# Optimization experiments

Hardware: AMD Instinct MI355X
Metric: run time of the kernel (lower is better)

The kernel has to match this reference:

```python
import jax, jax.numpy as jnp
import numpy as np


def setup_inputs() -> dict:
    key = jax.random.key(0)
    k1, k2, k3, k4, k5 = jax.random.split(key, 5)
    N, T, D, H = 64, 512, 512, 512
    std = 1.0 / np.sqrt(H)
    return {
        "x": jax.random.normal(k1, (N, T, D), dtype=jnp.float32),
        "weight_xh": jax.random.uniform(k2, (D, 4 * H), jnp.float32, -std, std),
        "weight_hh": jax.random.uniform(k3, (H, 4 * H), jnp.float32, -std, std),
        "bias_xh": jax.random.uniform(k4, (4 * H,), jnp.float32, -std, std),
        "bias_hh": jax.random.uniform(k5, (4 * H,), jnp.float32, -std, std),
    }


def reference(x, weight_xh, weight_hh, bias_xh, bias_hh):
    # x: (N, T, D) -> (T, N, D)
    x = jnp.transpose(x, (1, 0, 2))
    T, N, _ = x.shape
    H = weight_hh.shape[0]
    # Input projection for all timesteps at once: (T, N, 4H)
    xh = jnp.einsum("tnd,dk->tnk", x, weight_xh) + bias_xh

    def step(carry, xh_t):
        h_prev, c_prev = carry
        gates = xh_t + h_prev @ weight_hh + bias_hh  # (N, 4H)
        i = jax.nn.sigmoid(gates[:, 0:H])
        f = jax.nn.sigmoid(gates[:, H:2 * H])
        g = jnp.tanh(gates[:, 2 * H:3 * H])
        o = jax.nn.sigmoid(gates[:, 3 * H:4 * H])
        c = f * c_prev + i * g
        h = o * jnp.tanh(c)
        return (h, c), h

    h0 = jnp.zeros((N, H), dtype=x.dtype)
    c0 = jnp.zeros((N, H), dtype=x.dtype)
    _, y = jax.lax.scan(step, (h0, c0), xh)  # y: (T, N, H)
    return jnp.transpose(y, (1, 0, 2))  # (N, T, H)
```

## Files before the change

kernel.cpp:

```cpp
#include <hip/hip_runtime.h>

typedef unsigned short u16;
typedef unsigned int   u32;
typedef unsigned long long u64;
typedef __attribute__((ext_vector_type(8))) short short8;
typedef __attribute__((ext_vector_type(4))) float f32x4;

#define NB   64
#define TS   512
#define HD   512
#define RG   4
#define CG   16
#define NBLK (RG*CG)
#define HROW 256
#define SLOT (NB*HROW)

__device__ __forceinline__ u16 f2bf(float x) {
    union { float f; u32 i; } v; v.f = x;
    u32 r = (v.i + 0x7fffu + ((v.i >> 16) & 1u)) >> 16;
    return (u16)r;
}
__device__ __forceinline__ u32 pack2bf(float a, float b) {
    return (u32)f2bf(a) | ((u32)f2bf(b) << 16);
}
__device__ __forceinline__ float sigmf(float x) { return 1.0f / (1.0f + __expf(-x)); }
__device__ __forceinline__ float tanhf_fast(float x) { return 1.0f - 2.0f / (__expf(2.0f * x) + 1.0f); }

__global__ void cvt_x_k(const float* __restrict__ in, u16* __restrict__ out, int n) {
    int i = (blockIdx.x * blockDim.x + threadIdx.x) * 8;
    const int stride = gridDim.x * blockDim.x * 8;
    for (; i < n; i += stride) {
        const f32x4 a = *(const f32x4*)(in + i);
        const f32x4 b = *(const f32x4*)(in + i + 4);
        u32 q[4];
        q[0] = pack2bf(a[0], a[1]);
        q[1] = pack2bf(a[2], a[3]);
        q[2] = pack2bf(b[0], b[1]);
        q[3] = pack2bf(b[2], b[3]);
        *(f32x4*)(out + i) = *(f32x4*)q;
    }
}

__global__ void transpose_cvt_k(const float* __restrict__ in, u16* __restrict__ out,
                                int R, int C) {
    __shared__ float tile[32][33];
    const int c0 = blockIdx.x * 32;
    const int r0 = blockIdx.y * 32;
    const int tx = threadIdx.x & 31;
    const int ty = threadIdx.x >> 5;
#pragma unroll
    for (int i = 0; i < 32; i += 8)
        tile[ty + i][tx] = in[(size_t)(r0 + ty + i) * C + c0 + tx];
    __syncthreads();
#pragma unroll
    for (int i = 0; i < 32; i += 8)
        out[(size_t)(c0 + ty + i) * R + r0 + tx] = f2bf(tile[tx][ty + i]);
}

__global__ __launch_bounds__(512, 2) void lstm_fused(
    const u16*   __restrict__ xbg,
    const u16*   __restrict__ WtX,
    const u16*   __restrict__ WtH,
    const float* __restrict__ bxh,
    const float* __restrict__ bhh,
    u64*   __restrict__ hbuf,
    float* __restrict__ y)
{
    const int bid  = blockIdx.x;
    const int r    = bid & 3;
    const int cg   = bid >> 2;
    const int tid  = threadIdx.x;
    const int lane = tid & 63;
    const int wv   = tid >> 6;
    const int g    = wv & 3;
    const int kh   = wv >> 2;
    const int m15  = lane & 15;
    const int kq   = lane >> 4;
    const int n0   = r * 16;
    const int gcol0 = g * 512 + cg * 32;
    const int kbase = kh * 256;

    __shared__ __align__(16) u32 ldsH[16 * 256];
    __shared__ float gbuf2[2][4][16][34];

    short8 wx[2][8], wh[2][8];
#pragma unroll
    for (int c = 0; c < 2; ++c) {
        const u16* px = WtX + (size_t)(gcol0 + c * 16 + m15) * 512 + kbase + kq * 8;
        const u16* ph = WtH + (size_t)(gcol0 + c * 16 + m15) * 512 + kbase + kq * 8;
#pragma unroll
        for (int kc = 0; kc < 8; ++kc) {
            wx[c][kc] = *(const short8*)(px + kc * 32);
            wh[c][kc] = *(const short8*)(ph + kc * 32);
        }
    }

    const int erow = tid >> 5;
    const int ecol = tid & 31;
    const int hcol = cg * 32 + ecol;
    const float bI = bxh[hcol]        + bhh[hcol];
    const float bF = bxh[512  + hcol] + bhh[512  + hcol];
    const float bG = bxh[1024 + hcol] + bhh[1024 + hcol];
    const float bO = bxh[1536 + hcol] + bhh[1536 + hcol];
    float cst = 0.0f;

    const int lrow = 2 * wv + (lane >> 5);
    const int lq   = lane & 31;
    const int swzw = (lrow & 7) << 2;

    short8 xb[8];
    {
        const u16* xg = xbg + (size_t)(n0 + m15) * TS * HD + kbase + kq * 8;
#pragma unroll
        for (int kc = 0; kc < 8; ++kc) xb[kc] = *(const short8*)(xg + kc * 32);
    }

    for (int t = 0; t < TS; ++t) {
        u64 hq[8];
        const u64* gsrc = hbuf + (size_t)((t - 1) & 3) * SLOT
                        + (size_t)(n0 + lrow) * HROW + lq;
        if (t > 0) {
#pragma unroll
            for (int i = 0; i < 8; ++i)
                hq[i] = __hip_atomic_load(gsrc + i * 32, __ATOMIC_RELAXED,
                                          __HIP_MEMORY_SCOPE_AGENT);
        }

        f32x4 a00 = {0.f,0.f,0.f,0.f}, a01 = {0.f,0.f,0.f,0.f};
        f32x4 a10 = {0.f,0.f,0.f,0.f}, a11 = {0.f,0.f,0.f,0.f};
#pragma unroll
        for (int kc = 0; kc < 8; kc += 2) {
            a00 = __builtin_amdgcn_mfma_f32_16x16x32_bf16(xb[kc],   wx[0][kc],   a00, 0, 0, 0);
            a10 = __builtin_amdgcn_mfma_f32_16x16x32_bf16(xb[kc],   wx[1][kc],   a10, 0, 0, 0);
            a01 = __builtin_amdgcn_mfma_f32_16x16x32_bf16(xb[kc+1], wx[0][kc+1], a01, 0, 0, 0);
            a11 = __builtin_amdgcn_mfma_f32_16x16x32_bf16(xb[kc+1], wx[1][kc+1], a11, 0, 0, 0);
        }

        if (t > 0) {
            const u32 tagv = (u32)t;
            for (;;) {
                u32 stale = 0;
#pragma unroll
                for (int i = 0; i < 8; ++i) stale |= ((u32)hq[i]) ^ tagv;
                if (__all(stale == 0)) break;
                __builtin_amdgcn_s_sleep(1);
#pragma unroll
                for (int i = 0; i < 8; ++i)
                    hq[i] = __hip_atomic_load(gsrc + i * 32, __ATOMIC_RELAXED,
                                              __HIP_MEMORY_SCOPE_AGENT);
            }
#pragma unroll
            for (int i = 0; i < 8; ++i)
                ldsH[lrow * 256 + ((i * 32 + lq) ^ swzw)] = (u32)(hq[i] >> 32);
            __syncthreads();

            const u32* lbase = ldsH + m15 * 256;
            const int swzr = (m15 & 7) << 2;
#pragma unroll
            for (int kc = 0; kc < 8; kc += 2) {
                short8 h0 = *(const short8*)(lbase + (((kbase >> 1) + kc * 16 + kq * 4) ^ swzr));
                short8 h1 = *(const short8*)(lbase + (((kbase >> 1) + (kc + 1) * 16 + kq * 4) ^ swzr));
                a00 = __builtin_amdgcn_mfma_f32_16x16x32_bf16(h0, wh[0][kc],   a00, 0, 0, 0);
                a10 = __builtin_amdgcn_mfma_f32_16x16x32_bf16(h0, wh[1][kc],   a10, 0, 0, 0);
                a01 = __builtin_amdgcn_mfma_f32_16x16x32_bf16(h1, wh[0][kc+1], a01, 0, 0, 0);
                a11 = __builtin_amdgcn_mfma_f32_16x16x32_bf16(h1, wh[1][kc+1], a11, 0, 0, 0);
            }
        }

        {
            const f32x4 s0 = a00 + a01;
            const f32x4 s1 = a10 + a11;
#pragma unroll
            for (int j = 0; j < 4; ++j) {
                gbuf2[kh][g][kq * 4 + j][m15]      = s0[j];
                gbuf2[kh][g][kq * 4 + j][16 + m15] = s1[j];
            }
        }
        __syncthreads();

        {
            const float gi = gbuf2[0][0][erow][ecol] + gbuf2[1][0][erow][ecol] + bI;
            const float gf = gbuf2[0][1][erow][ecol] + gbuf2[1][1][erow][ecol] + bF;
            const float gg = gbuf2[0][2][erow][ecol] + gbuf2[1][2][erow][ecol] + bG;
            const float go = gbuf2[0][3][erow][ecol] + gbuf2[1][3][erow][ecol] + bO;
            const float iv = sigmf(gi);
            const float fv = sigmf(gf);
            const float gv = tanhf_fast(gg);
            const float ov = sigmf(go);
            cst = fv * cst + iv * gv;
            const float hv = ov * tanhf_fast(cst);
            y[((size_t)(n0 + erow) * TS + t) * HD + hcol] = hv;

            const u32 me = (u32)f2bf(hv);
            const u32 nb = (u32)__shfl_xor((int)me, 1);
            if ((ecol & 1) == 0) {
                const u64 v = ((u64)(me | (nb << 16)) << 32) | (u64)(u32)(t + 1);
                __hip_atomic_store(hbuf + (size_t)(t & 3) * SLOT
                                   + (size_t)(n0 + erow) * HROW + cg * 16 + (ecol >> 1),
                                   v, __ATOMIC_RELAXED, __HIP_MEMORY_SCOPE_AGENT);
            }
        }

        if (t + 1 < TS) {
            const u16* xg = xbg + ((size_t)(n0 + m15) * TS + (t + 1)) * HD + kbase + kq * 8;
#pragma unroll
            for (int kc = 0; kc < 8; ++kc) xb[kc] = *(const short8*)(xg + kc * 32);
        }
    }
}

extern "C" void kernel_launch(void* const* d_in, const int* in_sizes, int n_in,
                              void* d_out, int out_size, void* d_ws, size_t ws_size,
                              hipStream_t stream) {
    const float* x   = (const float*)d_in[0];
    const float* wxh = (const float*)d_in[1];
    const float* whh = (const float*)d_in[2];
    const float* bxh = (const float*)d_in[3];
    const float* bhh = (const float*)d_in[4];
    float* y = (float*)d_out;

    char* ws = (char*)d_ws;
    u64* hbuf = (u64*)ws;
    u16* WtX  = (u16*)(ws + (size_t)(1 << 19));
    u16* WtH  = (u16*)(ws + (size_t)(1 << 19) + (size_t)2048 * 512 * 2);
    u16* xbg  = (u16*)(ws + (size_t)(1 << 19) + (size_t)2 * 2048 * 512 * 2);

    (void)hipMemsetAsync(hbuf, 0, (size_t)4 * SLOT * sizeof(u64), stream);

    cvt_x_k<<<2048, 256, 0, stream>>>(x, xbg, NB * TS * HD);

    dim3 tgrid(2048 / 32, 512 / 32);
    transpose_cvt_k<<<tgrid, 256, 0, stream>>>(wxh, WtX, 512, 2048);
    transpose_cvt_k<<<tgrid, 256, 0, stream>>>(whh, WtH, 512, 2048);

    lstm_fused<<<dim3(NBLK), dim3(512), 0, stream>>>(xbg, WtX, WtH, bxh, bhh,
                                                     hbuf, y);
}
```

Measured before the change: 1.957 ms.

## Co-locate each batch-row chain on one XCC and poll hidden state through local cache

Launches an oversized grid of 1024 blocks. Each block reads its XCC id and claims a slot, so that each group of 16 column blocks sharing a batch-row chain sits on the same XCC; surplus blocks exit early. Producers also store h with sc0, and consumers poll with sc0 loads (a fast mode probed at t=1, with a periodic agent-scope fallback) to cut cross-die coherence latency on the per-step exchange. An epoch counter folded into the tags keeps stale buffers from earlier launches from matching. In exchange it adds block-claim overhead, extra stores and memsets, and relies on the XCC placement of co-resident blocks.

```diff
diff --git a/kernel.cpp b/kernel.cpp
--- a/kernel.cpp
+++ b/kernel.cpp
@@ -11,9 +11,10 @@
 #define HD   512
 #define RG   4
 #define CG   16
-#define NBLK (RG*CG)
+#define NGRID 1024
 #define HROW 256
 #define SLOT (NB*HROW)
+#define XCC_SIMM (20 | (3 << 11))
 
 __device__ __forceinline__ u16 f2bf(float x) {
     union { float f; u32 i; } v; v.f = x;
@@ -57,6 +58,39 @@
         out[(size_t)(c0 + ty + i) * R + r0 + tx] = f2bf(tile[tx][ty + i]);
 }
 
+__global__ void epoch_k(u32* e) {
+    __hip_atomic_fetch_add(e, 1u, __ATOMIC_RELAXED, __HIP_MEMORY_SCOPE_AGENT);
+}
+
+#define LOAD8_SC0(hq, p)                                                      \
+    asm volatile(                                                             \
+        "global_load_dwordx2 %0, %8, off sc0\n\t"                             \
+        "global_load_dwordx2 %1, %8, off offset:256 sc0\n\t"                  \
+        "global_load_dwordx2 %2, %8, off offset:512 sc0\n\t"                  \
+        "global_load_dwordx2 %3, %8, off offset:768 sc0\n\t"                  \
+        "global_load_dwordx2 %4, %8, off offset:1024 sc0\n\t"                 \
+        "global_load_dwordx2 %5, %8, off offset:1280 sc0\n\t"                 \
+        "global_load_dwordx2 %6, %8, off offset:1536 sc0\n\t"                 \
+        "global_load_dwordx2 %7, %8, off offset:1792 sc0\n\t"                 \
+        "s_waitcnt vmcnt(0)"                                                  \
+        : "=&v"(hq[0]), "=&v"(hq[1]), "=&v"(hq[2]), "=&v"(hq[3]),             \
+          "=&v"(hq[4]), "=&v"(hq[5]), "=&v"(hq[6]), "=&v"(hq[7])              \
+        : "v"(p) : "memory")
+
+__device__ __forceinline__ void load8_agent(u64* hq, const u64* p) {
+#pragma unroll
+    for (int i = 0; i < 8; ++i)
+        hq[i] = __hip_atomic_load(p + i * 32, __ATOMIC_RELAXED,
+                                  __HIP_MEMORY_SCOPE_AGENT);
+}
+
+__device__ __forceinline__ u32 tagmiss(const u64* hq, u32 tagv) {
+    u32 stale = 0;
+#pragma unroll
+    for (int i = 0; i < 8; ++i) stale |= ((u32)hq[i]) ^ tagv;
+    return stale;
+}
+
 __global__ __launch_bounds__(512, 2) void lstm_fused(
     const u16*   __restrict__ xbg,
     const u16*   __restrict__ WtX,
@@ -64,12 +98,47 @@
     const float* __restrict__ bxh,
     const float* __restrict__ bhh,
     u64*   __restrict__ hbuf,
-    float* __restrict__ y)
+    float* __restrict__ y,
+    u32*   __restrict__ epoch,
+    u32*   __restrict__ ctrl)
 {
-    const int bid  = blockIdx.x;
-    const int r    = bid & 3;
-    const int cg   = bid >> 2;
     const int tid  = threadIdx.x;
+    __shared__ u32 sClaim[3];
+    __shared__ __align__(16) u32 ldsH[16 * 256];
+    __shared__ float gbuf2[2][4][16][34];
+
+    if (tid == 0) {
+        const u32 key = __builtin_amdgcn_s_getreg(XCC_SIMM) & 7u;
+        u32* keySlot  = ctrl;
+        u32* chainCnt = ctrl + 8;
+        u32* chainTbl = ctrl + 16;
+        const u32 slot = __hip_atomic_fetch_add(keySlot + key, 1u,
+                                                __ATOMIC_RELAXED, __HIP_MEMORY_SCOPE_AGENT);
+        const u32 grp  = slot >> 4;
+        u32* entry = chainTbl + key * 64 + grp;
+        u32 ch;
+        if ((slot & 15u) == 0u) {
+            const u32 c = __hip_atomic_fetch_add(chainCnt, 1u,
+                                                 __ATOMIC_RELAXED, __HIP_MEMORY_SCOPE_AGENT);
+            ch = (c < RG) ? (c + 1u) : 0xFFFFFFFFu;
+            __hip_atomic_store(entry, ch, __ATOMIC_RELAXED, __HIP_MEMORY_SCOPE_AGENT);
+        } else {
+            do {
+                ch = __hip_atomic_load(entry, __ATOMIC_RELAXED, __HIP_MEMORY_SCOPE_AGENT);
+            } while (ch == 0u);
+        }
+        sClaim[0] = ch;
+        sClaim[1] = slot & 15u;
+        sClaim[2] = __hip_atomic_load(epoch, __ATOMIC_RELAXED, __HIP_MEMORY_SCOPE_AGENT);
+    }
+    __syncthreads();
+    const u32 chv = sClaim[0];
+    if (chv == 0xFFFFFFFFu) return;
+
+    const int r    = (int)chv - 1;
+    const int cg   = (int)sClaim[1];
+    const u32 tagbase = sClaim[2] << 10;
+
     const int lane = tid & 63;
     const int wv   = tid >> 6;
     const int g    = wv & 3;
@@ -80,9 +149,6 @@
     const int gcol0 = g * 512 + cg * 32;
     const int kbase = kh * 256;
 
-    __shared__ __align__(16) u32 ldsH[16 * 256];
-    __shared__ float gbuf2[2][4][16][34];
-
     short8 wx[2][8], wh[2][8];
 #pragma unroll
     for (int c = 0; c < 2; ++c) {
@@ -115,16 +181,13 @@
         for (int kc = 0; kc < 8; ++kc) xb[kc] = *(const short8*)(xg + kc * 32);
     }
 
+    int fastm = 0;
+
     for (int t = 0; t < TS; ++t) {
         u64 hq[8];
         const u64* gsrc = hbuf + (size_t)((t - 1) & 3) * SLOT
                         + (size_t)(n0 + lrow) * HROW + lq;
-        if (t > 0) {
-#pragma unroll
-            for (int i = 0; i < 8; ++i)
-                hq[i] = __hip_atomic_load(gsrc + i * 32, __ATOMIC_RELAXED,
-                                          __HIP_MEMORY_SCOPE_AGENT);
-        }
+        if (t > 0 && !fastm) load8_agent(hq, gsrc);
 
         f32x4 a00 = {0.f,0.f,0.f,0.f}, a01 = {0.f,0.f,0.f,0.f};
         f32x4 a10 = {0.f,0.f,0.f,0.f}, a11 = {0.f,0.f,0.f,0.f};
@@ -137,17 +200,34 @@
         }
 
         if (t > 0) {
-            const u32 tagv = (u32)t;
-            for (;;) {
-                u32 stale = 0;
-#pragma unroll
-                for (int i = 0; i < 8; ++i) stale |= ((u32)hq[i]) ^ tagv;
-                if (__all(stale == 0)) break;
-                __builtin_amdgcn_s_sleep(1);
-#pragma unroll
-                for (int i = 0; i < 8; ++i)
-                    hq[i] = __hip_atomic_load(gsrc + i * 32, __ATOMIC_RELAXED,
-                                              __HIP_MEMORY_SCOPE_AGENT);
+            const u32 tagv = tagbase | (u32)t;
+            if (fastm) {
+                int spins = 0;
+                for (;;) {
+                    LOAD8_SC0(hq, gsrc);
+                    if (__all(tagmiss(hq, tagv) == 0u)) break;
+                    ++spins;
+                    if ((spins & 255) == 0) {
+                        load8_agent(hq, gsrc);
+                        if (__all(tagmiss(hq, tagv) == 0u)) { fastm = 0; break; }
+                    }
+                    if (spins > 8) __builtin_amdgcn_s_sleep(1);
+                }
+            } else {
+                int spins = 0;
+                while (!__all(tagmiss(hq, tagv) == 0u)) {
+                    if (++spins > 4) __builtin_amdgcn_s_sleep(1);
+                    load8_agent(hq, gsrc);
+                }
+                if (t == 1) {
+                    u64 hp[8];
+                    int ok = 0;
+                    for (int pr = 0; pr < 8 && !ok; ++pr) {
+                        LOAD8_SC0(hp, gsrc);
+                        ok = __all(tagmiss(hp, tagv) == 0u);
+                    }
+                    fastm = ok;
+                }
             }
 #pragma unroll
             for (int i = 0; i < 8; ++i)
@@ -192,12 +272,15 @@
             y[((size_t)(n0 + erow) * TS + t) * HD + hcol] = hv;
 
             const u32 me = (u32)f2bf(hv);
-            const u32 nb = (u32)__shfl_xor((int)me, 1);
+            const u32 nb2 = (u32)__shfl_xor((int)me, 1);
             if ((ecol & 1) == 0) {
-                const u64 v = ((u64)(me | (nb << 16)) << 32) | (u64)(u32)(t + 1);
-                __hip_atomic_store(hbuf + (size_t)(t & 3) * SLOT
-                                   + (size_t)(n0 + erow) * HROW + cg * 16 + (ecol >> 1),
-                                   v, __ATOMIC_RELAXED, __HIP_MEMORY_SCOPE_AGENT);
+                const u64 v = ((u64)(me | (nb2 << 16)) << 32)
+                            | (u64)(tagbase | (u32)(t + 1));
+                u64* dst = hbuf + (size_t)(t & 3) * SLOT
+                         + (size_t)(n0 + erow) * HROW + cg * 16 + (ecol >> 1);
+                __hip_atomic_store(dst, v, __ATOMIC_RELAXED, __HIP_MEMORY_SCOPE_AGENT);
+                asm volatile("global_store_dwordx2 %0, %1, off sc0"
+                             :: "v"(dst), "v"(v) : "memory");
             }
         }
 
@@ -220,12 +303,16 @@
     float* y = (float*)d_out;
 
     char* ws = (char*)d_ws;
-    u64* hbuf = (u64*)ws;
-    u16* WtX  = (u16*)(ws + (size_t)(1 << 19));
-    u16* WtH  = (u16*)(ws + (size_t)(1 << 19) + (size_t)2048 * 512 * 2);
-    u16* xbg  = (u16*)(ws + (size_t)(1 << 19) + (size_t)2 * 2048 * 512 * 2);
-
-    (void)hipMemsetAsync(hbuf, 0, (size_t)4 * SLOT * sizeof(u64), stream);
+    u32* epoch = (u32*)ws;
+    u32* ctrl  = (u32*)(ws + 256);
+    u64* hbuf  = (u64*)(ws + 8192);
+    u16* WtX   = (u16*)(ws + 8192 + (size_t)4 * SLOT * 8);
+    u16* WtH   = (u16*)((char*)WtX + (size_t)2048 * 512 * 2);
+    u16* xbg   = (u16*)((char*)WtH + (size_t)2048 * 512 * 2);
+
+    epoch_k<<<1, 1, 0, stream>>>(epoch);
+    (void)hipMemsetAsync(ctrl, 0, 4096, stream);
+    (void)hipMemsetAsync(hbuf, 0, (size_t)4 * SLOT * 8, stream);
 
     cvt_x_k<<<2048, 256, 0, stream>>>(x, xbg, NB * TS * HD);
 
@@ -233,6 +320,6 @@
     transpose_cvt_k<<<tgrid, 256, 0, stream>>>(wxh, WtX, 512, 2048);
     transpose_cvt_k<<<tgrid, 256, 0, stream>>>(whh, WtH, 512, 2048);
 
-    lstm_fused<<<dim3(NBLK), dim3(512), 0, stream>>>(xbg, WtX, WtH, bxh, bhh,
-                                                     hbuf, y);
-}
+    lstm_fused<<<dim3(NGRID), dim3(512), 0, stream>>>(xbg, WtX, WtH, bxh, bhh,
+                                                      hbuf, y, epoch, ctrl);
+}
```

Result: slower. 2.267 ms (+15.8%).

## Restructure LSTM step so gates stay in registers and hbuf poll is prefetched

Applied to the files above, without the earlier changes.

Reorders the weight rows so each lane's MFMA output holds the i/f/g/o gates of the same hidden unit. This lets the elementwise LSTM update run directly on accumulators instead of going through an LDS gate buffer and an extra block barrier. Half the waves now issue the next step's hbuf poll loads early and pass partial sums through LDS behind a per-wave flag. The hidden-state LDS buffer is double-buffered so each step needs one barrier. An epoch counter is added to the tags so stale hbuf entries from earlier launches cannot match, at the cost of extra spin-wait logic and an added kernel launch.

```diff
diff --git a/kernel.cpp b/kernel.cpp
--- a/kernel.cpp
+++ b/kernel.cpp
@@ -57,6 +57,23 @@
         out[(size_t)(c0 + ty + i) * R + r0 + tx] = f2bf(tile[tx][ty + i]);
 }
 
+__global__ void epoch_k(u32* e) {
+    __hip_atomic_fetch_add(e, 1u, __ATOMIC_RELAXED, __HIP_MEMORY_SCOPE_AGENT);
+}
+
+__device__ __forceinline__ void load16_agent(u64* hq, const u64* p) {
+#pragma unroll
+    for (int i = 0; i < 16; ++i)
+        hq[i] = __hip_atomic_load(p + i * 16, __ATOMIC_RELAXED,
+                                  __HIP_MEMORY_SCOPE_AGENT);
+}
+__device__ __forceinline__ u32 tagmiss16(const u64* hq, u32 tagv) {
+    u32 stale = 0;
+#pragma unroll
+    for (int i = 0; i < 16; ++i) stale |= ((u32)hq[i]) ^ tagv;
+    return stale;
+}
+
 __global__ __launch_bounds__(512, 2) void lstm_fused(
     const u16*   __restrict__ xbg,
     const u16*   __restrict__ WtX,
@@ -64,7 +81,8 @@
     const float* __restrict__ bxh,
     const float* __restrict__ bhh,
     u64*   __restrict__ hbuf,
-    float* __restrict__ y)
+    float* __restrict__ y,
+    u32*   __restrict__ epoch)
 {
     const int bid  = blockIdx.x;
     const int r    = bid & 3;
@@ -72,41 +90,52 @@
     const int tid  = threadIdx.x;
     const int lane = tid & 63;
     const int wv   = tid >> 6;
-    const int g    = wv & 3;
+    const int p    = wv & 3;
     const int kh   = wv >> 2;
     const int m15  = lane & 15;
     const int kq   = lane >> 4;
     const int n0   = r * 16;
-    const int gcol0 = g * 512 + cg * 32;
     const int kbase = kh * 256;
 
-    __shared__ __align__(16) u32 ldsH[16 * 256];
-    __shared__ float gbuf2[2][4][16][34];
+    __shared__ __align__(16) u32 ldsH[2][16 * 256];
+    __shared__ f32x4 pbufA[4][64];
+    __shared__ f32x4 pbufB[4][64];
+    __shared__ u32 pflag[4];
+    __shared__ u32 sEpoch;
+
+    if (tid == 0)
+        sEpoch = __hip_atomic_load(epoch, __ATOMIC_RELAXED, __HIP_MEMORY_SCOPE_AGENT);
+    if (tid < 4) pflag[tid] = 0;
+    __syncthreads();
+    const u32 tagbase = sEpoch << 10;
 
     short8 wx[2][8], wh[2][8];
 #pragma unroll
-    for (int c = 0; c < 2; ++c) {
-        const u16* px = WtX + (size_t)(gcol0 + c * 16 + m15) * 512 + kbase + kq * 8;
-        const u16* ph = WtH + (size_t)(gcol0 + c * 16 + m15) * 512 + kbase + kq * 8;
+    for (int tt = 0; tt < 2; ++tt) {
+        const int gcolA = (m15 & 3) * 512 + cg * 32 + 8 * p + 4 * tt + (m15 >> 2);
+        const u16* px = WtX + (size_t)gcolA * 512 + kbase + kq * 8;
+        const u16* ph = WtH + (size_t)gcolA * 512 + kbase + kq * 8;
 #pragma unroll
         for (int kc = 0; kc < 8; ++kc) {
-            wx[c][kc] = *(const short8*)(px + kc * 32);
-            wh[c][kc] = *(const short8*)(ph + kc * 32);
-        }
-    }
-
-    const int erow = tid >> 5;
-    const int ecol = tid & 31;
-    const int hcol = cg * 32 + ecol;
-    const float bI = bxh[hcol]        + bhh[hcol];
-    const float bF = bxh[512  + hcol] + bhh[512  + hcol];
-    const float bG = bxh[1024 + hcol] + bhh[1024 + hcol];
-    const float bO = bxh[1536 + hcol] + bhh[1536 + hcol];
-    float cst = 0.0f;
-
-    const int lrow = 2 * wv + (lane >> 5);
-    const int lq   = lane & 31;
-    const int swzw = (lrow & 7) << 2;
+            wx[tt][kc] = *(const short8*)(px + kc * 32);
+            wh[tt][kc] = *(const short8*)(ph + kc * 32);
+        }
+    }
+
+    const int hc0 = cg * 32 + 8 * p + kq;
+    const float bI0 = bxh[hc0]        + bhh[hc0];
+    const float bF0 = bxh[512 + hc0]  + bhh[512 + hc0];
+    const float bG0 = bxh[1024 + hc0] + bhh[1024 + hc0];
+    const float bO0 = bxh[1536 + hc0] + bhh[1536 + hc0];
+    const float bI1 = bxh[hc0 + 4]        + bhh[hc0 + 4];
+    const float bF1 = bxh[512 + hc0 + 4]  + bhh[512 + hc0 + 4];
+    const float bG1 = bxh[1024 + hc0 + 4] + bhh[1024 + hc0 + 4];
+    const float bO1 = bxh[1536 + hc0 + 4] + bhh[1536 + hc0 + 4];
+    float c0st = 0.0f, c1st = 0.0f;
+
+    const int lrow4 = 4 * p + (lane >> 4);
+    const int lq    = lane & 15;
+    const int swzP  = (lrow4 & 7) << 2;
 
     short8 xb[8];
     {
@@ -115,96 +144,106 @@
         for (int kc = 0; kc < 8; ++kc) xb[kc] = *(const short8*)(xg + kc * 32);
     }
 
+    u64 hq[16];
+
     for (int t = 0; t < TS; ++t) {
-        u64 hq[8];
-        const u64* gsrc = hbuf + (size_t)((t - 1) & 3) * SLOT
-                        + (size_t)(n0 + lrow) * HROW + lq;
-        if (t > 0) {
-#pragma unroll
-            for (int i = 0; i < 8; ++i)
-                hq[i] = __hip_atomic_load(gsrc + i * 32, __ATOMIC_RELAXED,
-                                          __HIP_MEMORY_SCOPE_AGENT);
-        }
-
-        f32x4 a00 = {0.f,0.f,0.f,0.f}, a01 = {0.f,0.f,0.f,0.f};
-        f32x4 a10 = {0.f,0.f,0.f,0.f}, a11 = {0.f,0.f,0.f,0.f};
+        f32x4 A00 = {0.f,0.f,0.f,0.f}, A01 = {0.f,0.f,0.f,0.f};
+        f32x4 A10 = {0.f,0.f,0.f,0.f}, A11 = {0.f,0.f,0.f,0.f};
 #pragma unroll
         for (int kc = 0; kc < 8; kc += 2) {
-            a00 = __builtin_amdgcn_mfma_f32_16x16x32_bf16(xb[kc],   wx[0][kc],   a00, 0, 0, 0);
-            a10 = __builtin_amdgcn_mfma_f32_16x16x32_bf16(xb[kc],   wx[1][kc],   a10, 0, 0, 0);
-            a01 = __builtin_amdgcn_mfma_f32_16x16x32_bf16(xb[kc+1], wx[0][kc+1], a01, 0, 0, 0);
-            a11 = __builtin_amdgcn_mfma_f32_16x16x32_bf16(xb[kc+1], wx[1][kc+1], a11, 0, 0, 0);
-        }
-
-        if (t > 0) {
-            const u32 tagv = (u32)t;
-            for (;;) {
-                u32 stale = 0;
-#pragma unroll
-                for (int i = 0; i < 8; ++i) stale |= ((u32)hq[i]) ^ tagv;
-                if (__all(stale == 0)) break;
-                __builtin_amdgcn_s_sleep(1);
-#pragma unroll
-                for (int i = 0; i < 8; ++i)
-                    hq[i] = __hip_atomic_load(gsrc + i * 32, __ATOMIC_RELAXED,
-                                              __HIP_MEMORY_SCOPE_AGENT);
-            }
-#pragma unroll
-            for (int i = 0; i < 8; ++i)
-                ldsH[lrow * 256 + ((i * 32 + lq) ^ swzw)] = (u32)(hq[i] >> 32);
-            __syncthreads();
-
-            const u32* lbase = ldsH + m15 * 256;
-            const int swzr = (m15 & 7) << 2;
-#pragma unroll
-            for (int kc = 0; kc < 8; kc += 2) {
-                short8 h0 = *(const short8*)(lbase + (((kbase >> 1) + kc * 16 + kq * 4) ^ swzr));
-                short8 h1 = *(const short8*)(lbase + (((kbase >> 1) + (kc + 1) * 16 + kq * 4) ^ swzr));
-                a00 = __builtin_amdgcn_mfma_f32_16x16x32_bf16(h0, wh[0][kc],   a00, 0, 0, 0);
-                a10 = __builtin_amdgcn_mfma_f32_16x16x32_bf16(h0, wh[1][kc],   a10, 0, 0, 0);
-                a01 = __builtin_amdgcn_mfma_f32_16x16x32_bf16(h1, wh[0][kc+1], a01, 0, 0, 0);
-                a11 = __builtin_amdgcn_mfma_f32_16x16x32_bf16(h1, wh[1][kc+1], a11, 0, 0, 0);
-            }
-        }
-
-        {
-            const f32x4 s0 = a00 + a01;
-            const f32x4 s1 = a10 + a11;
-#pragma unroll
-            for (int j = 0; j < 4; ++j) {
-                gbuf2[kh][g][kq * 4 + j][m15]      = s0[j];
-                gbuf2[kh][g][kq * 4 + j][16 + m15] = s1[j];
-            }
-        }
-        __syncthreads();
-
-        {
-            const float gi = gbuf2[0][0][erow][ecol] + gbuf2[1][0][erow][ecol] + bI;
-            const float gf = gbuf2[0][1][erow][ecol] + gbuf2[1][1][erow][ecol] + bF;
-            const float gg = gbuf2[0][2][erow][ecol] + gbuf2[1][2][erow][ecol] + bG;
-            const float go = gbuf2[0][3][erow][ecol] + gbuf2[1][3][erow][ecol] + bO;
-            const float iv = sigmf(gi);
-            const float fv = sigmf(gf);
-            const float gv = tanhf_fast(gg);
-            const float ov = sigmf(go);
-            cst = fv * cst + iv * gv;
-            const float hv = ov * tanhf_fast(cst);
-            y[((size_t)(n0 + erow) * TS + t) * HD + hcol] = hv;
-
-            const u32 me = (u32)f2bf(hv);
-            const u32 nb = (u32)__shfl_xor((int)me, 1);
-            if ((ecol & 1) == 0) {
-                const u64 v = ((u64)(me | (nb << 16)) << 32) | (u64)(u32)(t + 1);
-                __hip_atomic_store(hbuf + (size_t)(t & 3) * SLOT
-                                   + (size_t)(n0 + erow) * HROW + cg * 16 + (ecol >> 1),
-                                   v, __ATOMIC_RELAXED, __HIP_MEMORY_SCOPE_AGENT);
-            }
+            A00 = __builtin_amdgcn_mfma_f32_16x16x32_bf16(wx[0][kc],   xb[kc],   A00, 0, 0, 0);
+            A10 = __builtin_amdgcn_mfma_f32_16x16x32_bf16(wx[1][kc],   xb[kc],   A10, 0, 0, 0);
+            A01 = __builtin_amdgcn_mfma_f32_16x16x32_bf16(wx[0][kc+1], xb[kc+1], A01, 0, 0, 0);
+            A11 = __builtin_amdgcn_mfma_f32_16x16x32_bf16(wx[1][kc+1], xb[kc+1], A11, 0, 0, 0);
         }
 
         if (t + 1 < TS) {
             const u16* xg = xbg + ((size_t)(n0 + m15) * TS + (t + 1)) * HD + kbase + kq * 8;
 #pragma unroll
             for (int kc = 0; kc < 8; ++kc) xb[kc] = *(const short8*)(xg + kc * 32);
+        }
+
+        if (kh == 1 && t > 0) {
+            const u64* gsrc = hbuf + (size_t)((t - 1) & 3) * SLOT
+                            + (size_t)(n0 + lrow4) * HROW + lq;
+            const u32 tagv = tagbase | (u32)t;
+            int spins = 0;
+            while (!__all(tagmiss16(hq, tagv) == 0u)) {
+                if (++spins > 6) __builtin_amdgcn_s_sleep(1);
+                load16_agent(hq, gsrc);
+            }
+            u32* lw = &ldsH[t & 1][lrow4 * 256];
+#pragma unroll
+            for (int i = 0; i < 16; ++i)
+                lw[(lq + 16 * i) ^ swzP] = (u32)(hq[i] >> 32);
+        }
+
+        __syncthreads();
+
+        if (t > 0) {
+            const u32* lb = &ldsH[t & 1][m15 * 256];
+            const int swzr = (m15 & 7) << 2;
+            const int b32 = kh * 128;
+#pragma unroll
+            for (int kc = 0; kc < 8; kc += 2) {
+                short8 h0 = *(const short8*)(lb + ((b32 + kc * 16 + kq * 4) ^ swzr));
+                short8 h1 = *(const short8*)(lb + ((b32 + (kc + 1) * 16 + kq * 4) ^ swzr));
+                A00 = __builtin_amdgcn_mfma_f32_16x16x32_bf16(wh[0][kc],   h0, A00, 0, 0, 0);
+                A10 = __builtin_amdgcn_mfma_f32_16x16x32_bf16(wh[1][kc],   h0, A10, 0, 0, 0);
+                A01 = __builtin_amdgcn_mfma_f32_16x16x32_bf16(wh[0][kc+1], h1, A01, 0, 0, 0);
+                A11 = __builtin_amdgcn_mfma_f32_16x16x32_bf16(wh[1][kc+1], h1, A11, 0, 0, 0);
+            }
+        }
+
+        if (kh == 1) {
+            if (t + 1 < TS) {
+                const u64* gsrc = hbuf + (size_t)(t & 3) * SLOT
+                                + (size_t)(n0 + lrow4) * HROW + lq;
+                load16_agent(hq, gsrc);
+            }
+            pbufA[p][lane] = A00 + A01;
+            pbufB[p][lane] = A10 + A11;
+            __hip_atomic_store(&pflag[p], (u32)(t + 1), __ATOMIC_RELEASE,
+                               __HIP_MEMORY_SCOPE_WORKGROUP);
+        } else {
+            int fs = 0;
+            while (__hip_atomic_load(&pflag[p], __ATOMIC_ACQUIRE,
+                                     __HIP_MEMORY_SCOPE_WORKGROUP) < (u32)(t + 1)) {
+                if (++fs > 16) __builtin_amdgcn_s_sleep(1);
+            }
+            const f32x4 g0 = A00 + A01 + pbufA[p][lane];
+            const f32x4 g1 = A10 + A11 + pbufB[p][lane];
+
+            const float i0 = sigmf(g0[0] + bI0);
+            const float f0 = sigmf(g0[1] + bF0);
+            const float gg0 = tanhf_fast(g0[2] + bG0);
+            const float o0 = sigmf(g0[3] + bO0);
+            c0st = f0 * c0st + i0 * gg0;
+            const float h0v = o0 * tanhf_fast(c0st);
+
+            const float i1 = sigmf(g1[0] + bI1);
+            const float f1 = sigmf(g1[1] + bF1);
+            const float gg1 = tanhf_fast(g1[2] + bG1);
+            const float o1 = sigmf(g1[3] + bO1);
+            c1st = f1 * c1st + i1 * gg1;
+            const float h1v = o1 * tanhf_fast(c1st);
+
+            const u32 me0 = (u32)f2bf(h0v);
+            const u32 me1 = (u32)f2bf(h1v);
+            const u32 nb0 = (u32)__shfl_xor((int)me0, 16);
+            const u32 nb1 = (u32)__shfl_xor((int)me1, 16);
+            if ((kq & 1) == 0) {
+                const u32 tg = tagbase | (u32)(t + 1);
+                const u64 v0 = ((u64)(me0 | (nb0 << 16)) << 32) | (u64)tg;
+                const u64 v1 = ((u64)(me1 | (nb1 << 16)) << 32) | (u64)tg;
+                u64* d0 = hbuf + (size_t)(t & 3) * SLOT
+                        + (size_t)(n0 + m15) * HROW + cg * 16 + 4 * p + (kq >> 1);
+                __hip_atomic_store(d0,     v0, __ATOMIC_RELAXED, __HIP_MEMORY_SCOPE_AGENT);
+                __hip_atomic_store(d0 + 2, v1, __ATOMIC_RELAXED, __HIP_MEMORY_SCOPE_AGENT);
+            }
+            float* yp = y + ((size_t)(n0 + m15) * TS + t) * HD + hc0;
+            yp[0] = h0v;
+            yp[4] = h1v;
         }
     }
 }
@@ -220,12 +259,14 @@
     float* y = (float*)d_out;
 
     char* ws = (char*)d_ws;
-    u64* hbuf = (u64*)ws;
-    u16* WtX  = (u16*)(ws + (size_t)(1 << 19));
-    u16* WtH  = (u16*)(ws + (size_t)(1 << 19) + (size_t)2048 * 512 * 2);
-    u16* xbg  = (u16*)(ws + (size_t)(1 << 19) + (size_t)2 * 2048 * 512 * 2);
-
-    (void)hipMemsetAsync(hbuf, 0, (size_t)4 * SLOT * sizeof(u64), stream);
+    u32* epoch = (u32*)ws;
+    u64* hbuf  = (u64*)(ws + 4096);
+    u16* WtX   = (u16*)(ws + 4096 + (size_t)4 * SLOT * 8);
+    u16* WtH   = (u16*)((char*)WtX + (size_t)2048 * 512 * 2);
+    u16* xbg   = (u16*)((char*)WtH + (size_t)2048 * 512 * 2);
+
+    epoch_k<<<1, 1, 0, stream>>>(epoch);
+    (void)hipMemsetAsync(hbuf, 0, (size_t)4 * SLOT * 8, stream);
 
     cvt_x_k<<<2048, 256, 0, stream>>>(x, xbg, NB * TS * HD);
 
@@ -234,5 +275,5 @@
     transpose_cvt_k<<<tgrid, 256, 0, stream>>>(whh, WtH, 512, 2048);
 
     lstm_fused<<<dim3(NBLK), dim3(512), 0, stream>>>(xbg, WtX, WtH, bxh, bhh,
-                                                     hbuf, y);
-}
+                                                     hbuf, y, epoch);
+}
```

Result: slower. 4.271 ms (+118.3%).
